# Optimization experiments

Hardware: AMD Instinct MI355X
Metric: run time of the kernel (lower is better)

The kernel has to match this reference:

```python
import jax, jax.numpy as jnp
import numpy as np

B, S, D, E = 32, 16, 64, 768  # batch, max summary segments, max doc splits, embed dim
EPS = 1e-12


def _l2norm(x):
    # tf.nn.l2_normalize: x * rsqrt(max(sum(x^2), eps))
    return x * jax.lax.rsqrt(jnp.maximum(jnp.sum(x * x, axis=-1, keepdims=True), EPS))


def setup_inputs() -> dict:
    key = jax.random.key(0)
    ks = jax.random.split(key, 12)
    nd = jax.random.randint(ks[0], (B,), 1, D + 1)
    ns = jax.random.randint(ks[1], (B,), 1, S + 1)
    doc = jax.random.normal(ks[2], (B, D, E), jnp.float32)
    seg = jax.random.normal(ks[3], (B, S, E), jnp.float32)
    # emulate RaggedTensor.to_tensor(): zero padding beyond ragged lengths
    doc = doc * (jnp.arange(D)[None, :, None] < nd[:, None, None])
    seg = seg * (jnp.arange(S)[None, :, None] < ns[:, None, None])
    tis = jax.random.uniform(ks[4], (B, S), jnp.float32)
    tis = jnp.where(jnp.arange(S)[None, :] < ns[:, None], tis, 1.0)
    tagg = jax.random.uniform(ks[5], (B,), jnp.float32)
    s1, s2, s3 = 1.0 / np.sqrt(2 * E), 1.0 / np.sqrt(E), 1.0 / np.sqrt(E // 2)
    W1 = jax.random.normal(ks[6], (2 * E, E), jnp.float32) * s1
    W2 = jax.random.normal(ks[7], (E, E // 2), jnp.float32) * s2
    W3 = jax.random.normal(ks[8], (E // 2, 1), jnp.float32) * s3
    return {
        'document_splits_embedding': doc,
        'summary_sentences_embedding': seg,
        'num_document_splits': nd,
        'num_summary_segments': ns,
        'target_agg_score': tagg,
        'target_instance_score': tis,
        'W1': W1, 'b1': jnp.zeros((E,), jnp.float32),
        'W2': W2, 'b2': jnp.zeros((E // 2,), jnp.float32),
        'W3': W3, 'b3': jnp.zeros((1,), jnp.float32),
    }


def reference(document_splits_embedding, summary_sentences_embedding,
              num_document_splits, num_summary_segments,
              target_agg_score, target_instance_score,
              W1, b1, W2, b2, W3, b3):
    doc, seg = document_splits_embedding, summary_sentences_embedding
    nd, ns = num_document_splits, num_summary_segments
    b, d, e = doc.shape
    s = seg.shape[1]
    nsf = ns.astype(jnp.float32)

    # target_instance_score padded with 1.0 beyond ragged length (done in setup; pass through)
    tis = target_instance_score

    # ---- pairwise MLP over all (segment, doc_split) pairs ----
    pair = jnp.concatenate([
        jnp.broadcast_to(doc[:, None, :, :], (b, s, d, e)),
        jnp.broadcast_to(seg[:, :, None, :], (b, s, d, e)),
    ], axis=-1)                                             # [B,S,D,2E]
    h = jax.nn.gelu(pair @ W1 + b1, approximate=False)      # [B,S,D,E]
    h = jax.nn.gelu(h @ W2 + b2, approximate=False)         # [B,S,D,E/2]
    mlp_out = jax.nn.sigmoid(h @ W3 + b3)[..., 0]           # [B,S,D]

    doc_mask = (jnp.arange(d)[None, :] < nd[:, None]).astype(jnp.float32)  # [B,D]
    scored = doc_mask[:, None, :] * mlp_out                # mask invalid doc splits
    pred0 = jnp.max(scored, axis=2)                         # [B,S]
    seg_scale = jnp.where(ns > 10, 1.0, 100.0)[:, None]     # faithful to mask+(1-mask)*100
    pred = seg_scale * pred0                                # [B,S]

    # ---- cosine similarity prior (keras CosineSimilarity = -cos) ----
    dn = _l2norm(doc)                                       # [B,D,E]
    sn = _l2norm(seg)                                       # [B,S,E]
    cos = jnp.einsum('bse,bde->bsd', sn, dn)                # [B,S,D]
    sim = doc_mask[:, None, :] * (1.0 + (-cos)) / 2.0
    doc_cos = jnp.max(sim, axis=2)                          # [B,S]
    seg_mask = (jnp.arange(s)[None, :] < ns[:, None]).astype(jnp.float32)
    diff = jnp.abs(doc_cos - pred) * seg_mask
    cos_prior = jnp.mean(jnp.sum(diff, axis=1) / nsf)

    # ---- correlation prior: Pearson correlation over the 768 'sample' axis ----
    c = seg - jnp.mean(seg, axis=-1, keepdims=True)
    z = c * jax.lax.rsqrt(jnp.maximum(jnp.sum(c * c, axis=-1, keepdims=True), EPS))
    R = (1.0 + jnp.einsum('bse,bte->bst', z, z)) / 2.0      # [B,S,S]
    p = pred
    t1 = (1.0 - p)[:, :, None] * (1.0 - p)[:, None, :]
    t2 = p[:, :, None] * p[:, None, :]
    pair_mask = seg_mask[:, :, None] * seg_mask[:, None, :]
    term = jnp.abs(t1 - R) * jnp.abs(t2 - R) * pair_mask
    corr_prior = jnp.mean(jnp.sum(term, axis=(1, 2)) / nsf)

    return (target_agg_score, tis, pred, ns, cos_prior, corr_prior)
```

## Files before the change

kernel.cpp:

```cpp
#include <hip/hip_runtime.h>
#include <hip/hip_bf16.h>
#include <math.h>

#define EPSF 1e-12f

typedef short bf16x8 __attribute__((ext_vector_type(8)));
typedef float f32x4  __attribute__((ext_vector_type(4)));

__device__ __forceinline__ float gelu_fast(float x) {
    float x2 = x * x;
    float z = -2.3021184f * x * fmaf(0.044715f, x2, 1.0f);
    float u = __builtin_amdgcn_exp2f(z);
    return x * __builtin_amdgcn_rcpf(1.0f + u);
}
__device__ __forceinline__ float sigmoid_fast(float x) {
    float u = __builtin_amdgcn_exp2f(-1.44269504f * x);
    return __builtin_amdgcn_rcpf(1.0f + u);
}
__device__ __forceinline__ float bf2f(unsigned short u) {
    return __uint_as_float(((unsigned int)u) << 16);
}
__device__ __forceinline__ unsigned short f2bf(float f) {
    unsigned int u = __float_as_uint(f);
    u += 0x7FFFu + ((u >> 16) & 1u);
    return (unsigned short)(u >> 16);
}

__global__ __launch_bounds__(256) void k_prep(
    const float* __restrict__ doc, const float* __restrict__ seg,
    const float* __restrict__ W1, const float* __restrict__ W2,
    float* __restrict__ dscale, float* __restrict__ sscale,
    float* __restrict__ smean, float* __restrict__ cscale,
    unsigned short* __restrict__ docB, unsigned short* __restrict__ segB,
    unsigned short* __restrict__ W1T, unsigned short* __restrict__ W2T)
{
    __shared__ float sT[64][65];
    int blk = blockIdx.x;
    int t = threadIdx.x;
    if (blk < 640) {
        int row = blk * 4 + (t >> 6);
        int lane = t & 63;
        const float* src = (row < 2048) ? (doc + (size_t)row * 768)
                                        : (seg + (size_t)(row - 2048) * 768);
        unsigned short* dst = (row < 2048) ? (docB + (size_t)row * 768)
                                           : (segB + (size_t)(row - 2048) * 768);
        float ss = 0.f, sm = 0.f;
        float xv[12];
        #pragma unroll
        for (int i = 0; i < 12; ++i) {
            float x = src[lane + 64 * i];
            xv[i] = x;
            ss += x * x; sm += x;
        }
        #pragma unroll
        for (int i = 0; i < 12; ++i) dst[lane + 64 * i] = f2bf(xv[i]);
        #pragma unroll
        for (int off = 32; off > 0; off >>= 1) {
            ss += __shfl_down(ss, off);
            sm += __shfl_down(sm, off);
        }
        if (lane == 0) {
            if (row < 2048) {
                dscale[row] = rsqrtf(fmaxf(ss, EPSF));
            } else {
                int r = row - 2048;
                sscale[r] = rsqrtf(fmaxf(ss, EPSF));
                float mean = sm * (1.0f / 768.0f);
                smean[r] = mean;
                cscale[r] = rsqrtf(fmaxf(ss - sm * mean, EPSF));
            }
        }
        return;
    }
    int tt = blk - 640;
    const float* in; unsigned short* out; int R, C, bx, by;
    if (tt < 288) { in = W1; out = W1T; R = 1536; C = 768; bx = tt % 12; by = tt / 12; }
    else { tt -= 288; in = W2; out = W2T; R = 768; C = 384; bx = tt % 6; by = tt / 6; }
    int c0 = bx * 64, r0 = by * 64;
    int tr = t >> 2, tc4 = (t & 3) * 16;
    #pragma unroll
    for (int i = 0; i < 4; ++i) {
        float4 v = *(const float4*)(in + (size_t)(r0 + tr) * C + c0 + tc4 + i * 4);
        sT[tr][tc4 + i * 4 + 0] = v.x; sT[tr][tc4 + i * 4 + 1] = v.y;
        sT[tr][tc4 + i * 4 + 2] = v.z; sT[tr][tc4 + i * 4 + 3] = v.w;
    }
    __syncthreads();
    union { uint4 v; unsigned short u[8]; } o0, o1;
    #pragma unroll
    for (int i = 0; i < 8; ++i) o0.u[i] = f2bf(sT[tc4 + i][tr]);
    #pragma unroll
    for (int i = 0; i < 8; ++i) o1.u[i] = f2bf(sT[tc4 + 8 + i][tr]);
    *(uint4*)(out + (size_t)(c0 + tr) * R + r0 + tc4) = o0.v;
    *(uint4*)(out + (size_t)(c0 + tr) * R + r0 + tc4 + 8) = o1.v;
}

__global__ __launch_bounds__(256) void k_l1(
    const unsigned short* __restrict__ docB, const unsigned short* __restrict__ segB,
    const unsigned short* __restrict__ W1T_bf, const float* __restrict__ b1,
    unsigned short* __restrict__ XdocB, unsigned short* __restrict__ XsegB)
{
    int mb = blockIdx.x;
    int n0 = blockIdx.y * 128;
    int t = threadIdx.x, w = t >> 6, l = t & 63;
    int lm = l & 15, kh = l >> 4;
    bool isdoc = (mb < 32);
    int m0 = isdoc ? mb * 64 : (mb - 32) * 64;
    const unsigned short* A = isdoc ? docB : segB;
    int koff = isdoc ? 0 : 768;
    unsigned short* C = isdoc ? XdocB : XsegB;

    const unsigned short* gA = A + (size_t)(m0 + lm) * 768 + kh * 8;
    const unsigned short* gB = W1T_bf + (size_t)(n0 + w * 32 + lm) * 1536 + koff + kh * 8;

    f32x4 acc[4][2];
    #pragma unroll
    for (int mt = 0; mt < 4; ++mt)
        #pragma unroll
        for (int nt = 0; nt < 2; ++nt) acc[mt][nt] = (f32x4){0.f, 0.f, 0.f, 0.f};

    bf16x8 aA[4], aB[4], bA[2], bB[2];
    #pragma unroll
    for (int mt = 0; mt < 4; ++mt) aA[mt] = *(const bf16x8*)(gA + (size_t)mt * 16 * 768);
    #pragma unroll
    for (int nt = 0; nt < 2; ++nt) bA[nt] = *(const bf16x8*)(gB + (size_t)nt * 16 * 1536);

    for (int kt = 0; kt < 12; ++kt) {
        int ko1 = kt * 64 + 32;
        #pragma unroll
        for (int mt = 0; mt < 4; ++mt) aB[mt] = *(const bf16x8*)(gA + (size_t)mt * 16 * 768 + ko1);
        #pragma unroll
        for (int nt = 0; nt < 2; ++nt) bB[nt] = *(const bf16x8*)(gB + (size_t)nt * 16 * 1536 + ko1);
        #pragma unroll
        for (int mt = 0; mt < 4; ++mt)
            #pragma unroll
            for (int nt = 0; nt < 2; ++nt)
                acc[mt][nt] = __builtin_amdgcn_mfma_f32_16x16x32_bf16(
                    aA[mt], bA[nt], acc[mt][nt], 0, 0, 0);
        if (kt < 11) {
            int ko2 = kt * 64 + 64;
            #pragma unroll
            for (int mt = 0; mt < 4; ++mt) aA[mt] = *(const bf16x8*)(gA + (size_t)mt * 16 * 768 + ko2);
            #pragma unroll
            for (int nt = 0; nt < 2; ++nt) bA[nt] = *(const bf16x8*)(gB + (size_t)nt * 16 * 1536 + ko2);
        }
        #pragma unroll
        for (int mt = 0; mt < 4; ++mt)
            #pragma unroll
            for (int nt = 0; nt < 2; ++nt)
                acc[mt][nt] = __builtin_amdgcn_mfma_f32_16x16x32_bf16(
                    aB[mt], bB[nt], acc[mt][nt], 0, 0, 0);
    }
    #pragma unroll
    for (int nt = 0; nt < 2; ++nt) {
        int n = n0 + w * 32 + nt * 16 + lm;
        float bv = isdoc ? 0.f : b1[n];
        #pragma unroll
        for (int mt = 0; mt < 4; ++mt)
            #pragma unroll
            for (int j = 0; j < 4; ++j) {
                int row = m0 + mt * 16 + kh * 4 + j;
                C[(size_t)row * 768 + n] = f2bf(acc[mt][nt][j] + bv);
            }
    }
}

__global__ __launch_bounds__(256, 2) void k_fused_mfma(
    const unsigned short* __restrict__ XdocB, const unsigned short* __restrict__ XsegB,
    const unsigned short* __restrict__ W2T_bf,
    const float* __restrict__ b2, const float* __restrict__ W3, const float* __restrict__ b3,
    const int* __restrict__ nd, const int* __restrict__ ns,
    float* __restrict__ out_pred, float* __restrict__ predv)
{
    __shared__ unsigned short sA0[64 * 64];
    __shared__ unsigned short sA1[64 * 64];
    __shared__ float sXseg[768];
    __shared__ float sRed[64][4];

    int bs = blockIdx.x;
    int b = bs >> 4;
    int t = threadIdx.x, w = t >> 6, l = t & 63;
    int lm = l & 15, kh = l >> 4, sw2 = (lm & 7) << 4;

    for (int i = t; i < 768; i += 256) sXseg[i] = bf2f(XsegB[(size_t)bs * 768 + i]);

    const int ndb = nd[b];
    const float segscale = (ns[b] > 10) ? 1.0f : 100.0f;
    const float b3v = b3[0];

    f32x4 acc[4][6];
    #pragma unroll
    for (int mt = 0; mt < 4; ++mt)
        #pragma unroll
        for (int nt = 0; nt < 6; ++nt) acc[mt][nt] = (f32x4){0.f, 0.f, 0.f, 0.f};

    int ar = t >> 2, ak = (t & 3) * 16;
    int asw = (ar & 7) << 4;
    const char* gXd = (const char*)XdocB + (size_t)(b * 64 + ar) * 1536;
    const unsigned short* gW2w = W2T_bf + (size_t)(w * 96 + lm) * 768 + kh * 8;

    union u128 { uint4 v; unsigned short u[8]; };

    bf16x8 bbA[6], bbB[6];
    #pragma unroll
    for (int nt = 0; nt < 6; ++nt)
        bbA[nt] = *(const bf16x8*)(gW2w + (size_t)nt * 16 * 768);

    u128 xc0, xc1;
    xc0.v = *(const uint4*)(gXd + ak * 2);
    xc1.v = *(const uint4*)(gXd + ak * 2 + 16);
    __syncthreads();
    {
        u128 o0, o1;
        #pragma unroll
        for (int i = 0; i < 8; ++i)
            o0.u[i] = f2bf(gelu_fast(bf2f(xc0.u[i]) + sXseg[ak + i]));
        #pragma unroll
        for (int i = 0; i < 8; ++i)
            o1.u[i] = f2bf(gelu_fast(bf2f(xc1.u[i]) + sXseg[ak + 8 + i]));
        *(uint4*)((char*)sA0 + ar * 128 + ((ak * 2) ^ asw)) = o0.v;
        *(uint4*)((char*)sA0 + ar * 128 + ((ak * 2 + 16) ^ asw)) = o1.v;
    }

    #pragma unroll
    for (int kt = 0; kt < 12; ++kt) {
        unsigned short* cbuf = (kt & 1) ? sA1 : sA0;
        unsigned short* nbuf = (kt & 1) ? sA0 : sA1;
        __syncthreads();
        u128 xn0, xn1;
        if (kt < 11) {
            xn0.v = *(const uint4*)(gXd + (kt + 1) * 128 + ak * 2);
            xn1.v = *(const uint4*)(gXd + (kt + 1) * 128 + ak * 2 + 16);
        }
        {
            #pragma unroll
            for (int nt = 0; nt < 6; ++nt)
                bbB[nt] = *(const bf16x8*)(gW2w + (size_t)nt * 16 * 768 + kt * 64 + 32);
            int kb = (kh * 16) ^ sw2;
            bf16x8 a[4];
            #pragma unroll
            for (int mt = 0; mt < 4; ++mt)
                a[mt] = *(const bf16x8*)((const char*)cbuf + (mt * 16 + lm) * 128 + kb);
            #pragma unroll
            for (int mt = 0; mt < 4; ++mt)
                #pragma unroll
                for (int nt = 0; nt < 6; ++nt)
                    acc[mt][nt] = __builtin_amdgcn_mfma_f32_16x16x32_bf16(
                        a[mt], bbA[nt], acc[mt][nt], 0, 0, 0);
        }
        {
            if (kt < 11) {
                #pragma unroll
                for (int nt = 0; nt < 6; ++nt)
                    bbA[nt] = *(const bf16x8*)(gW2w + (size_t)nt * 16 * 768 + (kt + 1) * 64);
            }
            int kb = (64 + kh * 16) ^ sw2;
            bf16x8 a[4];
            #pragma unroll
            for (int mt = 0; mt < 4; ++mt)
                a[mt] = *(const bf16x8*)((const char*)cbuf + (mt * 16 + lm) * 128 + kb);
            #pragma unroll
            for (int mt = 0; mt < 4; ++mt)
                #pragma unroll
                for (int nt = 0; nt < 6; ++nt)
                    acc[mt][nt] = __builtin_amdgcn_mfma_f32_16x16x32_bf16(
                        a[mt], bbB[nt], acc[mt][nt], 0, 0, 0);
        }
        if (kt < 11) {
            u128 o0, o1;
            #pragma unroll
            for (int i = 0; i < 8; ++i)
                o0.u[i] = f2bf(gelu_fast(bf2f(xn0.u[i]) + sXseg[(kt + 1) * 64 + ak + i]));
            #pragma unroll
            for (int i = 0; i < 8; ++i)
                o1.u[i] = f2bf(gelu_fast(bf2f(xn1.u[i]) + sXseg[(kt + 1) * 64 + ak + 8 + i]));
            *(uint4*)((char*)nbuf + ar * 128 + ((ak * 2) ^ asw)) = o0.v;
            *(uint4*)((char*)nbuf + ar * 128 + ((ak * 2 + 16) ^ asw)) = o1.v;
        }
    }

    float b2v[6], w3v[6];
    #pragma unroll
    for (int nt = 0; nt < 6; ++nt) {
        int n = w * 96 + nt * 16 + lm;
        b2v[nt] = b2[n]; w3v[nt] = W3[n];
    }
    #pragma unroll
    for (int mt = 0; mt < 4; ++mt) {
        #pragma unroll
        for (int j = 0; j < 4; ++j) {
            float s = 0.f;
            #pragma unroll
            for (int nt = 0; nt < 6; ++nt)
                s += gelu_fast(acc[mt][nt][j] + b2v[nt]) * w3v[nt];
            s += __shfl_xor(s, 1); s += __shfl_xor(s, 2);
            s += __shfl_xor(s, 4); s += __shfl_xor(s, 8);
            if (lm == 0) sRed[mt * 16 + kh * 4 + j][w] = s;
        }
    }
    __syncthreads();
    if (w == 0) {
        float h3 = sRed[l][0] + sRed[l][1] + sRed[l][2] + sRed[l][3] + b3v;
        float sig = sigmoid_fast(h3);
        float val = (l < ndb) ? sig : 0.f;
        #pragma unroll
        for (int off = 32; off > 0; off >>= 1) val = fmaxf(val, __shfl_xor(val, off));
        if (l == 0) {
            float pv = segscale * val;
            out_pred[bs] = pv;
            predv[bs] = pv;
        }
    }
}

__global__ __launch_bounds__(256) void k_post(
    const unsigned short* __restrict__ docB, const unsigned short* __restrict__ segB,
    const float* __restrict__ seg,
    const float* __restrict__ dscale, const float* __restrict__ sscale,
    const float* __restrict__ smean, const float* __restrict__ cscale,
    const int* __restrict__ nd, const int* __restrict__ ns,
    const float* __restrict__ predv,
    float* __restrict__ diffs, float* __restrict__ corrb)
{
    __shared__ float sZ[16][772];
    __shared__ float sRedC[16][4];
    __shared__ float sPred[16];
    __shared__ float wsum[4];
    int blk = blockIdx.x;
    int t = threadIdx.x;

    if (blk < 32) {
        int b = blk;
        int w = t >> 6, l = t & 63;
        int lm = l & 15, kh = l >> 4;
        const unsigned short* gS = segB + (size_t)(b * 16 + lm) * 768 + kh * 8;
        const unsigned short* gD = docB + (size_t)(b * 64 + w * 16 + lm) * 768 + kh * 8;
        f32x4 acc = (f32x4){0.f, 0.f, 0.f, 0.f};
        for (int kt = 0; kt < 24; ++kt) {
            bf16x8 a = *(const bf16x8*)(gS + kt * 32);
            bf16x8 bb = *(const bf16x8*)(gD + kt * 32);
            acc = __builtin_amdgcn_mfma_f32_16x16x32_bf16(a, bb, acc, 0, 0, 0);
        }
        int ndb = nd[b];
        int d = w * 16 + lm;
        float dsc = dscale[b * 64 + d];
        #pragma unroll
        for (int j = 0; j < 4; ++j) {
            int s = kh * 4 + j;
            float cosv = acc[j] * sscale[b * 16 + s] * dsc;
            float sim = (d < ndb) ? (1.0f - cosv) * 0.5f : 0.f;
            sim = fmaxf(sim, __shfl_xor(sim, 1));
            sim = fmaxf(sim, __shfl_xor(sim, 2));
            sim = fmaxf(sim, __shfl_xor(sim, 4));
            sim = fmaxf(sim, __shfl_xor(sim, 8));
            if (lm == 0) sRedC[s][w] = sim;
        }
        __syncthreads();
        if (t < 16) {
            float dc = fmaxf(fmaxf(sRedC[t][0], sRedC[t][1]),
                             fmaxf(sRedC[t][2], sRedC[t][3]));
            float diff = fabsf(dc - predv[b * 16 + t]);
            diffs[b * 16 + t] = (t < ns[b]) ? diff : 0.f;
        }
        return;
    }

    int b = blk - 32;
    if (t < 16) sPred[t] = predv[b * 16 + t];
    for (int i = t; i < 16 * 768; i += 256) {
        int s = i / 768; int e = i - s * 768;
        sZ[s][e] = (seg[((size_t)b * 16 + s) * 768 + e] - smean[b * 16 + s]) * cscale[b * 16 + s];
    }
    __syncthreads();
    int s = t >> 4, tt = t & 15;
    const float4* z1 = (const float4*)&sZ[s][0];
    const float4* z2 = (const float4*)&sZ[tt][0];
    float dot = 0.f;
    #pragma unroll 4
    for (int e = 0; e < 192; ++e) {
        float4 a = z1[e], c = z2[e];
        dot += a.x * c.x + a.y * c.y + a.z * c.z + a.w * c.w;
    }
    float R = 0.5f * (1.0f + dot);
    int nsb = ns[b];
    float ps = sPred[s], pt = sPred[tt];
    float t1 = (1.f - ps) * (1.f - pt), t2 = ps * pt;
    float term = (s < nsb && tt < nsb) ? fabsf(t1 - R) * fabsf(t2 - R) : 0.f;
    #pragma unroll
    for (int off = 32; off > 0; off >>= 1) term += __shfl_down(term, off);
    int lane = t & 63, w = t >> 6;
    if (lane == 0) wsum[w] = term;
    __syncthreads();
    if (t == 0) corrb[b] = (wsum[0] + wsum[1] + wsum[2] + wsum[3]) / (float)nsb;
}

__global__ __launch_bounds__(256) void k_final(
    const float* __restrict__ tagg, const float* __restrict__ tis,
    const int* __restrict__ ns, const float* __restrict__ diffs,
    const float* __restrict__ corrb, float* __restrict__ out)
{
    int t = threadIdx.x;
    if (t < 32) out[t] = tagg[t];
    out[32 + t] = tis[t];
    out[32 + 256 + t] = tis[256 + t];
    if (t < 32) out[1056 + t] = (float)ns[t];
    float l1 = 0.f, l2 = 0.f;
    if (t < 32) {
        float sb = 0.f;
        #pragma unroll
        for (int s2 = 0; s2 < 16; ++s2) sb += diffs[t * 16 + s2];
        l1 = sb / (float)ns[t];
        l2 = corrb[t];
    }
    #pragma unroll
    for (int off = 16; off > 0; off >>= 1) {
        l1 += __shfl_down(l1, off);
        l2 += __shfl_down(l2, off);
    }
    if (t == 0) { out[1088] = l1 * (1.0f / 32.0f); out[1089] = l2 * (1.0f / 32.0f); }
}

extern "C" void kernel_launch(void* const* d_in, const int* in_sizes, int n_in,
                              void* d_out, int out_size, void* d_ws, size_t ws_size,
                              hipStream_t stream)
{
    const float* doc  = (const float*)d_in[0];
    const float* seg  = (const float*)d_in[1];
    const int*   nd   = (const int*)d_in[2];
    const int*   ns   = (const int*)d_in[3];
    const float* tagg = (const float*)d_in[4];
    const float* tis  = (const float*)d_in[5];
    const float* W1   = (const float*)d_in[6];
    const float* b1   = (const float*)d_in[7];
    const float* W2   = (const float*)d_in[8];
    const float* b2   = (const float*)d_in[9];
    const float* W3   = (const float*)d_in[10];
    const float* b3   = (const float*)d_in[11];
    float* out = (float*)d_out;

    float* fws      = (float*)d_ws;
    float* dscale   = fws;
    float* sscale   = dscale + 2048;
    float* smean    = sscale + 512;
    float* cscale   = smean + 512;
    float* predv    = cscale + 512;
    float* diffs    = predv + 512;
    float* corrb    = diffs + 512;
    unsigned short* docB  = (unsigned short*)(corrb + 32);
    unsigned short* segB  = docB + (size_t)2048 * 768;
    unsigned short* W1T   = segB + (size_t)512 * 768;
    unsigned short* W2T   = W1T + (size_t)768 * 1536;
    unsigned short* XdocB = W2T + (size_t)384 * 768;
    unsigned short* XsegB = XdocB + (size_t)2048 * 768;

    k_prep<<<1000, 256, 0, stream>>>(doc, seg, W1, W2, dscale, sscale, smean,
                                     cscale, docB, segB, W1T, W2T);
    k_l1<<<dim3(40, 6), 256, 0, stream>>>(docB, segB, W1T, b1, XdocB, XsegB);
    k_fused_mfma<<<512, 256, 0, stream>>>(XdocB, XsegB, W2T, b2, W3, b3, nd, ns,
                                          out + 544, predv);
    k_post<<<64, 256, 0, stream>>>(docB, segB, seg, dscale, sscale, smean,
                                   cscale, nd, ns, predv, diffs, corrb);
    k_final<<<1, 256, 0, stream>>>(tagg, tis, ns, diffs, corrb, out);
}
```

Baseline: 87.08 us.

## Fold post-processing into fused MLP kernel and drop a launch

Removes the separate k_post launch. Its cosine-max work and its Pearson correlation matrix now run as 64 extra blocks of the fused MLP kernel, sharing one union of shared memory. The correlation matmul now uses bf16 MFMA instead of fp32 FMA loops. The pred-dependent diff and correlation terms move into k_final, and the pass-through output copies move into an extra block of k_prep. The goal is to cut one kernel launch and its serialization gap and to overlap the small post work with the main MLP. The cost is extra workspace traffic and slightly lower precision in the correlation dot products.

```diff
diff --git a/kernel.cpp b/kernel.cpp
--- a/kernel.cpp
+++ b/kernel.cpp
@@ -29,14 +29,24 @@
 __global__ __launch_bounds__(256) void k_prep(
     const float* __restrict__ doc, const float* __restrict__ seg,
     const float* __restrict__ W1, const float* __restrict__ W2,
+    const float* __restrict__ tagg, const float* __restrict__ tis,
+    const int* __restrict__ ns,
     float* __restrict__ dscale, float* __restrict__ sscale,
     float* __restrict__ smean, float* __restrict__ cscale,
     unsigned short* __restrict__ docB, unsigned short* __restrict__ segB,
-    unsigned short* __restrict__ W1T, unsigned short* __restrict__ W2T)
+    unsigned short* __restrict__ W1T, unsigned short* __restrict__ W2T,
+    float* __restrict__ out)
 {
     __shared__ float sT[64][65];
     int blk = blockIdx.x;
     int t = threadIdx.x;
+    if (blk == 1000) {
+        if (t < 32) out[t] = tagg[t];
+        out[32 + t] = tis[t];
+        out[32 + 256 + t] = tis[256 + t];
+        if (t < 32) out[1056 + t] = (float)ns[t];
+        return;
+    }
     if (blk < 640) {
         int row = blk * 4 + (t >> 6);
         int lane = t & 63;
@@ -73,9 +83,9 @@
         return;
     }
     int tt = blk - 640;
-    const float* in; unsigned short* out; int R, C, bx, by;
-    if (tt < 288) { in = W1; out = W1T; R = 1536; C = 768; bx = tt % 12; by = tt / 12; }
-    else { tt -= 288; in = W2; out = W2T; R = 768; C = 384; bx = tt % 6; by = tt / 6; }
+    const float* in; unsigned short* out2; int R, C, bx, by;
+    if (tt < 288) { in = W1; out2 = W1T; R = 1536; C = 768; bx = tt % 12; by = tt / 12; }
+    else { tt -= 288; in = W2; out2 = W2T; R = 768; C = 384; bx = tt % 6; by = tt / 6; }
     int c0 = bx * 64, r0 = by * 64;
     int tr = t >> 2, tc4 = (t & 3) * 16;
     #pragma unroll
@@ -90,8 +100,8 @@
     for (int i = 0; i < 8; ++i) o0.u[i] = f2bf(sT[tc4 + i][tr]);
     #pragma unroll
     for (int i = 0; i < 8; ++i) o1.u[i] = f2bf(sT[tc4 + 8 + i][tr]);
-    *(uint4*)(out + (size_t)(c0 + tr) * R + r0 + tc4) = o0.v;
-    *(uint4*)(out + (size_t)(c0 + tr) * R + r0 + tc4 + 8) = o1.v;
+    *(uint4*)(out2 + (size_t)(c0 + tr) * R + r0 + tc4) = o0.v;
+    *(uint4*)(out2 + (size_t)(c0 + tr) * R + r0 + tc4 + 8) = o1.v;
 }
 
 __global__ __launch_bounds__(256) void k_l1(
@@ -169,19 +179,89 @@
     const unsigned short* __restrict__ W2T_bf,
     const float* __restrict__ b2, const float* __restrict__ W3, const float* __restrict__ b3,
     const int* __restrict__ nd, const int* __restrict__ ns,
-    float* __restrict__ out_pred, float* __restrict__ predv)
+    const unsigned short* __restrict__ docB, const unsigned short* __restrict__ segB,
+    const float* __restrict__ seg,
+    const float* __restrict__ dscale, const float* __restrict__ sscale,
+    const float* __restrict__ smean, const float* __restrict__ cscale,
+    float* __restrict__ out_pred, float* __restrict__ predv,
+    float* __restrict__ dcws, float* __restrict__ Rws)
 {
-    __shared__ unsigned short sA0[64 * 64];
-    __shared__ unsigned short sA1[64 * 64];
-    __shared__ float sXseg[768];
-    __shared__ float sRed[64][4];
-
-    int bs = blockIdx.x;
+    __shared__ union {
+        struct {
+            unsigned short sA0[64 * 64];
+            unsigned short sA1[64 * 64];
+            float sXseg[768];
+            float sRed[64][4];
+        } p;
+        struct { float sRedC[16][4]; } c;
+        struct { unsigned short zb[16][776]; } r;
+    } U;
+
+    int blk = blockIdx.x;
+    int t = threadIdx.x, w = t >> 6, l = t & 63;
+    int lm = l & 15, kh = l >> 4;
+
+    if (blk >= 512) {
+        if (blk < 544) {
+            int b = blk - 512;
+            const unsigned short* gS = segB + (size_t)(b * 16 + lm) * 768 + kh * 8;
+            const unsigned short* gD = docB + (size_t)(b * 64 + w * 16 + lm) * 768 + kh * 8;
+            f32x4 acc = (f32x4){0.f, 0.f, 0.f, 0.f};
+            for (int kt = 0; kt < 24; ++kt) {
+                bf16x8 a = *(const bf16x8*)(gS + kt * 32);
+                bf16x8 bb = *(const bf16x8*)(gD + kt * 32);
+                acc = __builtin_amdgcn_mfma_f32_16x16x32_bf16(a, bb, acc, 0, 0, 0);
+            }
+            int ndb = nd[b];
+            int d = w * 16 + lm;
+            float dsc = dscale[b * 64 + d];
+            #pragma unroll
+            for (int j = 0; j < 4; ++j) {
+                int s = kh * 4 + j;
+                float cosv = acc[j] * sscale[b * 16 + s] * dsc;
+                float sim = (d < ndb) ? (1.0f - cosv) * 0.5f : 0.f;
+                sim = fmaxf(sim, __shfl_xor(sim, 1));
+                sim = fmaxf(sim, __shfl_xor(sim, 2));
+                sim = fmaxf(sim, __shfl_xor(sim, 4));
+                sim = fmaxf(sim, __shfl_xor(sim, 8));
+                if (lm == 0) U.c.sRedC[s][w] = sim;
+            }
+            __syncthreads();
+            if (t < 16) {
+                float dc = fmaxf(fmaxf(U.c.sRedC[t][0], U.c.sRedC[t][1]),
+                                 fmaxf(U.c.sRedC[t][2], U.c.sRedC[t][3]));
+                dcws[b * 16 + t] = dc;
+            }
+        } else {
+            int b = blk - 544;
+            for (int i = t; i < 16 * 768; i += 256) {
+                int s = i / 768; int e = i - s * 768;
+                U.r.zb[s][e] = f2bf((seg[((size_t)b * 16 + s) * 768 + e]
+                                     - smean[b * 16 + s]) * cscale[b * 16 + s]);
+            }
+            __syncthreads();
+            if (w == 0) {
+                f32x4 acc = (f32x4){0.f, 0.f, 0.f, 0.f};
+                #pragma unroll
+                for (int kt = 0; kt < 24; ++kt) {
+                    bf16x8 z = *(const bf16x8*)&U.r.zb[lm][kt * 32 + kh * 8];
+                    acc = __builtin_amdgcn_mfma_f32_16x16x32_bf16(z, z, acc, 0, 0, 0);
+                }
+                #pragma unroll
+                for (int j = 0; j < 4; ++j) {
+                    int row = kh * 4 + j;
+                    Rws[b * 256 + row * 16 + lm] = 0.5f * (1.0f + acc[j]);
+                }
+            }
+        }
+        return;
+    }
+
+    int bs = blk;
     int b = bs >> 4;
-    int t = threadIdx.x, w = t >> 6, l = t & 63;
-    int lm = l & 15, kh = l >> 4, sw2 = (lm & 7) << 4;
-
-    for (int i = t; i < 768; i += 256) sXseg[i] = bf2f(XsegB[(size_t)bs * 768 + i]);
+    int sw2 = (lm & 7) << 4;
+
+    for (int i = t; i < 768; i += 256) U.p.sXseg[i] = bf2f(XsegB[(size_t)bs * 768 + i]);
 
     const int ndb = nd[b];
     const float segscale = (ns[b] > 10) ? 1.0f : 100.0f;
@@ -205,26 +285,26 @@
     for (int nt = 0; nt < 6; ++nt)
         bbA[nt] = *(const bf16x8*)(gW2w + (size_t)nt * 16 * 768);
 
-    u128 xc0, xc1;
-    xc0.v = *(const uint4*)(gXd + ak * 2);
-    xc1.v = *(const uint4*)(gXd + ak * 2 + 16);
-    __syncthreads();
     {
+        u128 xc0, xc1;
+        xc0.v = *(const uint4*)(gXd + ak * 2);
+        xc1.v = *(const uint4*)(gXd + ak * 2 + 16);
+        __syncthreads();
         u128 o0, o1;
         #pragma unroll
         for (int i = 0; i < 8; ++i)
-            o0.u[i] = f2bf(gelu_fast(bf2f(xc0.u[i]) + sXseg[ak + i]));
+            o0.u[i] = f2bf(gelu_fast(bf2f(xc0.u[i]) + U.p.sXseg[ak + i]));
         #pragma unroll
         for (int i = 0; i < 8; ++i)
-            o1.u[i] = f2bf(gelu_fast(bf2f(xc1.u[i]) + sXseg[ak + 8 + i]));
-        *(uint4*)((char*)sA0 + ar * 128 + ((ak * 2) ^ asw)) = o0.v;
-        *(uint4*)((char*)sA0 + ar * 128 + ((ak * 2 + 16) ^ asw)) = o1.v;
+            o1.u[i] = f2bf(gelu_fast(bf2f(xc1.u[i]) + U.p.sXseg[ak + 8 + i]));
+        *(uint4*)((char*)U.p.sA0 + ar * 128 + ((ak * 2) ^ asw)) = o0.v;
+        *(uint4*)((char*)U.p.sA0 + ar * 128 + ((ak * 2 + 16) ^ asw)) = o1.v;
     }
 
     #pragma unroll
     for (int kt = 0; kt < 12; ++kt) {
-        unsigned short* cbuf = (kt & 1) ? sA1 : sA0;
-        unsigned short* nbuf = (kt & 1) ? sA0 : sA1;
+        unsigned short* cbuf = (kt & 1) ? U.p.sA1 : U.p.sA0;
+        unsigned short* nbuf = (kt & 1) ? U.p.sA0 : U.p.sA1;
         __syncthreads();
         u128 xn0, xn1;
         if (kt < 11) {
@@ -269,10 +349,10 @@
             u128 o0, o1;
             #pragma unroll
             for (int i = 0; i < 8; ++i)
-                o0.u[i] = f2bf(gelu_fast(bf2f(xn0.u[i]) + sXseg[(kt + 1) * 64 + ak + i]));
+                o0.u[i] = f2bf(gelu_fast(bf2f(xn0.u[i]) + U.p.sXseg[(kt + 1) * 64 + ak + i]));
             #pragma unroll
             for (int i = 0; i < 8; ++i)
-                o1.u[i] = f2bf(gelu_fast(bf2f(xn1.u[i]) + sXseg[(kt + 1) * 64 + ak + 8 + i]));
+                o1.u[i] = f2bf(gelu_fast(bf2f(xn1.u[i]) + U.p.sXseg[(kt + 1) * 64 + ak + 8 + i]));
             *(uint4*)((char*)nbuf + ar * 128 + ((ak * 2) ^ asw)) = o0.v;
             *(uint4*)((char*)nbuf + ar * 128 + ((ak * 2 + 16) ^ asw)) = o1.v;
         }
@@ -294,12 +374,12 @@
                 s += gelu_fast(acc[mt][nt][j] + b2v[nt]) * w3v[nt];
             s += __shfl_xor(s, 1); s += __shfl_xor(s, 2);
             s += __shfl_xor(s, 4); s += __shfl_xor(s, 8);
-            if (lm == 0) sRed[mt * 16 + kh * 4 + j][w] = s;
+            if (lm == 0) U.p.sRed[mt * 16 + kh * 4 + j][w] = s;
         }
     }
     __syncthreads();
     if (w == 0) {
-        float h3 = sRed[l][0] + sRed[l][1] + sRed[l][2] + sRed[l][3] + b3v;
+        float h3 = U.p.sRed[l][0] + U.p.sRed[l][1] + U.p.sRed[l][2] + U.p.sRed[l][3] + b3v;
         float sig = sigmoid_fast(h3);
         float val = (l < ndb) ? sig : 0.f;
         #pragma unroll
@@ -312,111 +392,50 @@
     }
 }
 
-__global__ __launch_bounds__(256) void k_post(
-    const unsigned short* __restrict__ docB, const unsigned short* __restrict__ segB,
-    const float* __restrict__ seg,
-    const float* __restrict__ dscale, const float* __restrict__ sscale,
-    const float* __restrict__ smean, const float* __restrict__ cscale,
-    const int* __restrict__ nd, const int* __restrict__ ns,
-    const float* __restrict__ predv,
-    float* __restrict__ diffs, float* __restrict__ corrb)
+__global__ __launch_bounds__(256) void k_final(
+    const int* __restrict__ ns, const float* __restrict__ dcws,
+    const float* __restrict__ Rws, const float* __restrict__ predv,
+    float* __restrict__ out)
 {
-    __shared__ float sZ[16][772];
-    __shared__ float sRedC[16][4];
-    __shared__ float sPred[16];
-    __shared__ float wsum[4];
-    int blk = blockIdx.x;
+    __shared__ float sl1[32], sl2[32];
     int t = threadIdx.x;
-
-    if (blk < 32) {
-        int b = blk;
-        int w = t >> 6, l = t & 63;
-        int lm = l & 15, kh = l >> 4;
-        const unsigned short* gS = segB + (size_t)(b * 16 + lm) * 768 + kh * 8;
-        const unsigned short* gD = docB + (size_t)(b * 64 + w * 16 + lm) * 768 + kh * 8;
-        f32x4 acc = (f32x4){0.f, 0.f, 0.f, 0.f};
-        for (int kt = 0; kt < 24; ++kt) {
-            bf16x8 a = *(const bf16x8*)(gS + kt * 32);
-            bf16x8 bb = *(const bf16x8*)(gD + kt * 32);
-            acc = __builtin_amdgcn_mfma_f32_16x16x32_bf16(a, bb, acc, 0, 0, 0);
-        }
-        int ndb = nd[b];
-        int d = w * 16 + lm;
-        float dsc = dscale[b * 64 + d];
-        #pragma unroll
-        for (int j = 0; j < 4; ++j) {
-            int s = kh * 4 + j;
-            float cosv = acc[j] * sscale[b * 16 + s] * dsc;
-            float sim = (d < ndb) ? (1.0f - cosv) * 0.5f : 0.f;
-            sim = fmaxf(sim, __shfl_xor(sim, 1));
-            sim = fmaxf(sim, __shfl_xor(sim, 2));
-            sim = fmaxf(sim, __shfl_xor(sim, 4));
-            sim = fmaxf(sim, __shfl_xor(sim, 8));
-            if (lm == 0) sRedC[s][w] = sim;
-        }
-        __syncthreads();
-        if (t < 16) {
-            float dc = fmaxf(fmaxf(sRedC[t][0], sRedC[t][1]),
-                             fmaxf(sRedC[t][2], sRedC[t][3]));
-            float diff = fabsf(dc - predv[b * 16 + t]);
-            diffs[b * 16 + t] = (t < ns[b]) ? diff : 0.f;
-        }
-        return;
-    }
-
-    int b = blk - 32;
-    if (t < 16) sPred[t] = predv[b * 16 + t];
-    for (int i = t; i < 16 * 768; i += 256) {
-        int s = i / 768; int e = i - s * 768;
-        sZ[s][e] = (seg[((size_t)b * 16 + s) * 768 + e] - smean[b * 16 + s]) * cscale[b * 16 + s];
+    if (t < 32) {
+        int nsb = ns[t];
+        float sb = 0.f;
+        #pragma unroll
+        for (int s = 0; s < 16; ++s) {
+            float d = fabsf(dcws[t * 16 + s] - predv[t * 16 + s]);
+            sb += (s < nsb) ? d : 0.f;
+        }
+        sl1[t] = sb / (float)nsb;
+    }
+    {
+        int b = t >> 3, c = t & 7;
+        int nsb = ns[b];
+        float sum = 0.f;
+        #pragma unroll
+        for (int k = 0; k < 32; ++k) {
+            int idx = c * 32 + k;
+            int s = idx >> 4, tt = idx & 15;
+            float R = Rws[b * 256 + idx];
+            float ps = predv[b * 16 + s], pt = predv[b * 16 + tt];
+            float t1 = (1.f - ps) * (1.f - pt), t2 = ps * pt;
+            float term = fabsf(t1 - R) * fabsf(t2 - R);
+            sum += (s < nsb && tt < nsb) ? term : 0.f;
+        }
+        sum += __shfl_xor(sum, 1);
+        sum += __shfl_xor(sum, 2);
+        sum += __shfl_xor(sum, 4);
+        if (c == 0) sl2[b] = sum / (float)nsb;
     }
     __syncthreads();
-    int s = t >> 4, tt = t & 15;
-    const float4* z1 = (const float4*)&sZ[s][0];
-    const float4* z2 = (const float4*)&sZ[tt][0];
-    float dot = 0.f;
-    #pragma unroll 4
-    for (int e = 0; e < 192; ++e) {
-        float4 a = z1[e], c = z2[e];
-        dot += a.x * c.x + a.y * c.y + a.z * c.z + a.w * c.w;
-    }
-    float R = 0.5f * (1.0f + dot);
-    int nsb = ns[b];
-    float ps = sPred[s], pt = sPred[tt];
-    float t1 = (1.f - ps) * (1.f - pt), t2 = ps * pt;
-    float term = (s < nsb && tt < nsb) ? fabsf(t1 - R) * fabsf(t2 - R) : 0.f;
-    #pragma unroll
-    for (int off = 32; off > 0; off >>= 1) term += __shfl_down(term, off);
-    int lane = t & 63, w = t >> 6;
-    if (lane == 0) wsum[w] = term;
-    __syncthreads();
-    if (t == 0) corrb[b] = (wsum[0] + wsum[1] + wsum[2] + wsum[3]) / (float)nsb;
-}
-
-__global__ __launch_bounds__(256) void k_final(
-    const float* __restrict__ tagg, const float* __restrict__ tis,
-    const int* __restrict__ ns, const float* __restrict__ diffs,
-    const float* __restrict__ corrb, float* __restrict__ out)
-{
-    int t = threadIdx.x;
-    if (t < 32) out[t] = tagg[t];
-    out[32 + t] = tis[t];
-    out[32 + 256 + t] = tis[256 + t];
-    if (t < 32) out[1056 + t] = (float)ns[t];
-    float l1 = 0.f, l2 = 0.f;
-    if (t < 32) {
-        float sb = 0.f;
-        #pragma unroll
-        for (int s2 = 0; s2 < 16; ++s2) sb += diffs[t * 16 + s2];
-        l1 = sb / (float)ns[t];
-        l2 = corrb[t];
-    }
-    #pragma unroll
-    for (int off = 16; off > 0; off >>= 1) {
-        l1 += __shfl_down(l1, off);
-        l2 += __shfl_down(l2, off);
-    }
-    if (t == 0) { out[1088] = l1 * (1.0f / 32.0f); out[1089] = l2 * (1.0f / 32.0f); }
+    if (t == 0) {
+        float a = 0.f, bsum = 0.f;
+        #pragma unroll
+        for (int i = 0; i < 32; ++i) { a += sl1[i]; bsum += sl2[i]; }
+        out[1088] = a * (1.0f / 32.0f);
+        out[1089] = bsum * (1.0f / 32.0f);
+    }
 }
 
 extern "C" void kernel_launch(void* const* d_in, const int* in_sizes, int n_in,
@@ -443,21 +462,22 @@
     float* smean    = sscale + 512;
     float* cscale   = smean + 512;
     float* predv    = cscale + 512;
-    float* diffs    = predv + 512;
-    float* corrb    = diffs + 512;
-    unsigned short* docB  = (unsigned short*)(corrb + 32);
+    float* dcws     = predv + 512;
+    float* Rws      = dcws + 512;
+    unsigned short* docB  = (unsigned short*)(Rws + 8192);
     unsigned short* segB  = docB + (size_t)2048 * 768;
     unsigned short* W1T   = segB + (size_t)512 * 768;
     unsigned short* W2T   = W1T + (size_t)768 * 1536;
     unsigned short* XdocB = W2T + (size_t)384 * 768;
     unsigned short* XsegB = XdocB + (size_t)2048 * 768;
 
-    k_prep<<<1000, 256, 0, stream>>>(doc, seg, W1, W2, dscale, sscale, smean,
-                                     cscale, docB, segB, W1T, W2T);
+    k_prep<<<1001, 256, 0, stream>>>(doc, seg, W1, W2, tagg, tis, ns,
+                                     dscale, sscale, smean, cscale,
+                                     docB, segB, W1T, W2T, out);
     k_l1<<<dim3(40, 6), 256, 0, stream>>>(docB, segB, W1T, b1, XdocB, XsegB);
-    k_fused_mfma<<<512, 256, 0, stream>>>(XdocB, XsegB, W2T, b2, W3, b3, nd, ns,
-                                          out + 544, predv);
-    k_post<<<64, 256, 0, stream>>>(docB, segB, seg, dscale, sscale, smean,
-                                   cscale, nd, ns, predv, diffs, corrb);
-    k_final<<<1, 256, 0, stream>>>(tagg, tis, ns, diffs, corrb, out);
-}
+    k_fused_mfma<<<576, 256, 0, stream>>>(XdocB, XsegB, W2T, b2, W3, b3, nd, ns,
+                                          docB, segB, seg, dscale, sscale,
+                                          smean, cscale, out + 544, predv,
+                                          dcws, Rws);
+    k_final<<<1, 256, 0, stream>>>(ns, dcws, Rws, predv, out);
+}
```

Measured after the change: 83.98 us. 1.04x faster.
